# Performance work log

Measured on AMD Instinct MI355X. Metric: run time of the kernel, lower is better.

The kernel has to match this reference:

```python
import jax, jax.numpy as jnp
import numpy as np

GRID = 128  # grid_size from init_kwargs


def _splat(coords2, alpha, feats):
    """Alpha-weighted splat of per-point features onto a GRIDxGRID plane.
    coords2: [N,2] normalized coords in [-1,1]; alpha: [N]; feats: [N,C].
    Returns [C, GRID, GRID].
    """
    g = ((coords2 * 0.5 + 0.5) * (GRID - 1)).astype(jnp.int32)  # trunc like torch .long()
    g = jnp.clip(g, 0, GRID - 1)
    idx = g[:, 0] * GRID + g[:, 1]  # [N]
    num = jax.ops.segment_sum(feats * alpha[:, None], idx, num_segments=GRID * GRID)  # [G2,C]
    den = jnp.maximum(jax.ops.segment_sum(alpha, idx, num_segments=GRID * GRID), 1e-6)  # [G2]
    C = feats.shape[-1]
    return (num / den[:, None]).T.reshape(C, GRID, GRID)


def setup_inputs() -> dict:
    key = jax.random.key(0)
    k1, _ = jax.random.split(key)
    B, N, C = 4, 131072, 196
    GS_feats = jax.random.normal(k1, (B, N, C), dtype=jnp.float32)
    scene_bounds = jnp.arange(6, dtype=jnp.float32)  # (0,1,2,3,4,5) -> unit extents
    return {"GS_feats": GS_feats, "scene_bounds": scene_bounds}


def reference(GS_feats, scene_bounds):
    lo = scene_bounds[jnp.array([0, 2, 4])]  # [3]
    hi = scene_bounds[jnp.array([1, 3, 5])]  # [3]
    coords_n = 2.0 * (GS_feats[..., :3] - lo) / (hi - lo) - 1.0  # [B,N,3]
    feats = jnp.concatenate([coords_n, GS_feats[..., 3:]], axis=-1)  # [B,N,C]
    alpha = jax.nn.sigmoid(feats[..., 3])  # [B,N]
    # plane coord pairs: xy, xz, yz -> [B,3,N,2]
    plane_coords = jnp.stack(
        [coords_n[..., jnp.array([0, 1])],
         coords_n[..., jnp.array([0, 2])],
         coords_n[..., jnp.array([1, 2])]], axis=1)
    splat_planes = jax.vmap(_splat, in_axes=(0, None, None))  # over the 3 planes
    splat_batch = jax.vmap(splat_planes, in_axes=(0, 0, 0))   # over batch
    return splat_batch(plane_coords, alpha, feats)  # [B,3,C,GRID,GRID]
```

## Files before the change

kernel.cpp:

```cpp
#include <hip/hip_runtime.h>
#include <math.h>

#define GRID_SZ 128
#define NC 196
#define NC4 49
#define G2 (GRID_SZ*GRID_SZ)
#define BPB 64
#define SLOTS 128
#define SLOTF 200
#define AW 16


__device__ __forceinline__ void lds_flush(float* __restrict__ tbl, int tag,
                                          float v0, float v1, float v2, float v3,
                                          float d, int lane, bool l4) {
    float* slot = tbl + tag * SLOTF;
    atomicAdd(slot + lane, v0);
    atomicAdd(slot + 64 + lane, v1);
    atomicAdd(slot + 128 + lane, v2);
    if (l4) atomicAdd(slot + 192 + lane, v3);
    if (lane == 4) atomicAdd(slot + 196, d);
}

__global__ __launch_bounds__(1024, 1) void lds_accum_kernel(
    const float* __restrict__ gs, const float* __restrict__ sb,
    float* __restrict__ nw, float* __restrict__ dn,
    float* __restrict__ tblout, int N) {
    __shared__ float tbl[SLOTS * SLOTF];

    const int tid = threadIdx.x;
    const int lane = tid & 63;
    const int widx = tid >> 6;

    for (int i = tid; i < SLOTS * SLOTF; i += 1024) tbl[i] = 0.f;
    __syncthreads();

    const int b = blockIdx.x / BPB;
    const int blk = blockIdx.x % BPB;
    const int strip = N / BPB;
    const int cnt = strip / AW;
    const long long p0 = (long long)b * N + (long long)blk * strip
                       + (long long)widx * cnt;

    const float lo0 = sb[0], hi0 = sb[1];
    const float lo1 = sb[2], hi1 = sb[3];
    const float lo2 = sb[4], hi2 = sb[5];
    const float s0 = 2.0f / (hi0 - lo0);
    const float s1 = 2.0f / (hi1 - lo1);
    const float s2 = 2.0f / (hi2 - lo2);

    const float* rows = gs + (size_t)p0 * NC;
    const bool l4 = (lane < 4);

    #define LOADP(J, V0, V1, V2, V3)                                   \
        {                                                              \
            const float* r_ = rows + (size_t)(J) * NC;                 \
            V0 = r_[lane];                                             \
            V1 = r_[64 + lane];                                        \
            V2 = r_[128 + lane];                                       \
            V3 = l4 ? r_[192 + lane] : 0.f;                            \
        }

    float a0, a1, a2, a3, b0, b1, b2, b3;
    float c0_, c1_, c2_, c3_, d0, d1, d2, d3;
    {
        const int i1 = (cnt > 1) ? 1 : 0;
        const int i2 = (cnt > 2) ? 2 : 0;
        const int i3 = (cnt > 3) ? 3 : 0;
        LOADP(0, a0, a1, a2, a3);
        LOADP(i1, b0, b1, b2, b3);
        LOADP(i2, c0_, c1_, c2_, c3_);
        LOADP(i3, d0, d1, d2, d3);
    }

    float z0 = 0.f, z1 = 0.f, z2 = 0.f, z3 = 0.f, zd = 0.f;
    float y0 = 0.f, y1 = 0.f, y2 = 0.f, y3 = 0.f, yd = 0.f;
    int ctag = -1;
    float cc0 = 0.f, cc1 = 0.f, cc2 = 0.f, cc3 = 0.f, ccd = 0.f;

    #define CONSUME(V0, V1, V2, V3)                                          \
        {                                                                    \
            const float hx = __shfl(V0, 0);                                  \
            const float hy = __shfl(V0, 1);                                  \
            const float hz = __shfl(V0, 2);                                  \
            const float hw = __shfl(V0, 3);                                  \
            const float cnx = (hx - lo0) * s0 - 1.0f;                        \
            const float cny = (hy - lo1) * s1 - 1.0f;                        \
            const float cnz = (hz - lo2) * s2 - 1.0f;                        \
            int gx = (int)((cnx * 0.5f + 0.5f) * 127.0f);                    \
            int gy = (int)((cny * 0.5f + 0.5f) * 127.0f);                    \
            int gz = (int)((cnz * 0.5f + 0.5f) * 127.0f);                    \
            gx = min(127, max(0, gx));                                       \
            gy = min(127, max(0, gy));                                       \
            gz = min(127, max(0, gz));                                       \
            const float alpha = 1.0f / (1.0f + __expf(-hw));                 \
            float v0 = V0;                                                   \
            if (lane == 0) v0 = cnx;                                         \
            else if (lane == 1) v0 = cny;                                    \
            else if (lane == 2) v0 = cnz;                                    \
            const float av0 = v0 * alpha;                                    \
            const float av1 = (V1) * alpha;                                  \
            const float av2 = (V2) * alpha;                                  \
            const float av3 = (V3) * alpha;                                  \
            if ((gy | gz) == 0) {                                            \
                if (gx == 0) {                                               \
                    z0 += av0; z1 += av1; z2 += av2; z3 += av3; zd += alpha; \
                } else if (gx == 127) {                                      \
                    y0 += av0; y1 += av1; y2 += av2; y3 += av3; yd += alpha; \
                } else if (gx == ctag) {                                     \
                    cc0 += av0; cc1 += av1; cc2 += av2; cc3 += av3;          \
                    ccd += alpha;                                            \
                } else {                                                     \
                    if (ctag > 0)                                            \
                        lds_flush(tbl, ctag, cc0, cc1, cc2, cc3, ccd,        \
                                  lane, l4);                                 \
                    ctag = gx;                                               \
                    cc0 = av0; cc1 = av1; cc2 = av2; cc3 = av3;              \
                    ccd = alpha;                                             \
                }                                                            \
            } else {                                                         \
                const int cells[3] = { gx * GRID_SZ + gy, gx * GRID_SZ + gz, \
                                       gy * GRID_SZ + gz };                  \
                _Pragma("unroll")                                            \
                for (int p = 0; p < 3; ++p) {                                \
                    const int bin = (b * 3 + p) * G2 + cells[p];             \
                    float* dst = nw + (size_t)bin * NC;                      \
                    unsafeAtomicAdd(dst + lane, av0);                        \
                    unsafeAtomicAdd(dst + 64 + lane, av1);                   \
                    unsafeAtomicAdd(dst + 128 + lane, av2);                  \
                    if (l4) unsafeAtomicAdd(dst + 192 + lane, av3);          \
                    if (lane == 4) unsafeAtomicAdd(dn + bin, alpha);         \
                }                                                            \
            }                                                                \
        }

    for (int j = 0; j < cnt; j += 4) {
        float e0, e1, e2, e3, f0, f1, f2, f3;
        float g0, g1, g2, g3, h0, h1, h2, h3;
        const int j4 = (j + 4 < cnt) ? j + 4 : cnt - 1;
        const int j5 = (j + 5 < cnt) ? j + 5 : cnt - 1;
        const int j6 = (j + 6 < cnt) ? j + 6 : cnt - 1;
        const int j7 = (j + 7 < cnt) ? j + 7 : cnt - 1;
        LOADP(j4, e0, e1, e2, e3);
        LOADP(j5, f0, f1, f2, f3);
        LOADP(j6, g0, g1, g2, g3);
        LOADP(j7, h0, h1, h2, h3);

        CONSUME(a0, a1, a2, a3);
        CONSUME(b0, b1, b2, b3);
        CONSUME(c0_, c1_, c2_, c3_);
        CONSUME(d0, d1, d2, d3);

        a0 = e0; a1 = e1; a2 = e2; a3 = e3;
        b0 = f0; b1 = f1; b2 = f2; b3 = f3;
        c0_ = g0; c1_ = g1; c2_ = g2; c3_ = g3;
        d0 = h0; d1 = h1; d2 = h2; d3 = h3;
    }
    #undef CONSUME
    #undef LOADP

    if (ctag > 0) lds_flush(tbl, ctag, cc0, cc1, cc2, cc3, ccd, lane, l4);
    lds_flush(tbl, 127, y0, y1, y2, y3, yd, lane, l4);
    lds_flush(tbl, 0, z0, z1, z2, z3, zd, lane, l4);

    __syncthreads();
    for (int i = tid; i < SLOTS * SLOTF; i += 1024) {
        const int s = i / SLOTF;
        const int f = i - s * SLOTF;
        tblout[(((size_t)b * SLOTS + s) * BPB + blk) * SLOTF + f] = tbl[i];
    }
}


__global__ __launch_bounds__(256) void table_reduce_kernel(
    const float* __restrict__ tblout,
    float* __restrict__ nw, float* __restrict__ dn, int B) {
    const int lane = threadIdx.x & 63;
    const int w = blockIdx.x * 4 + (threadIdx.x >> 6);
    if (w >= B * SLOTS) return;
    const int b = w >> 7;
    const int gx = w & 127;
    const bool l4 = (lane < 4);

    const float* base = tblout + ((size_t)(b * SLOTS + gx) * BPB) * SLOTF;
    float a0 = 0.f, a1 = 0.f, a2 = 0.f, a3 = 0.f, den = 0.f;
    for (int r = 0; r < BPB; ++r) {
        const float* rec = base + (size_t)r * SLOTF;
        a0 += rec[lane];
        a1 += rec[64 + lane];
        a2 += rec[128 + lane];
        if (l4) a3 += rec[192 + lane];
        if (lane == 4) den += rec[196];
    }

    const int cells[3] = { gx * GRID_SZ, gx * GRID_SZ, 0 };
    #pragma unroll
    for (int p = 0; p < 3; ++p) {
        const int bin = (b * 3 + p) * G2 + cells[p];
        float* dst = nw + (size_t)bin * NC;
        unsafeAtomicAdd(dst + lane, a0);
        unsafeAtomicAdd(dst + 64 + lane, a1);
        unsafeAtomicAdd(dst + 128 + lane, a2);
        if (l4) unsafeAtomicAdd(dst + 192 + lane, a3);
        if (lane == 4) unsafeAtomicAdd(dn + bin, den);
    }
}


#define TCELLS 64
__global__ __launch_bounds__(256) void xpose_kernel(const float* __restrict__ nw,
                                                    const float* __restrict__ dn,
                                                    float* __restrict__ out) {
    __shared__ float tile[TCELLS][197];
    __shared__ float dinv[TCELLS];
    const int t = threadIdx.x;
    const int pg = blockIdx.x >> 8;
    const int c0 = (blockIdx.x & 255) * TCELLS;

    const float* src = nw + ((size_t)pg * G2 + c0) * NC;
    for (int i = t; i < TCELLS * NC4; i += 256) {
        const int cell = i / NC4;
        const int cp = i - cell * NC4;
        float4 v = ((const float4*)(src + (size_t)cell * NC))[cp];
        float* dst = &tile[cell][cp * 4];
        dst[0] = v.x; dst[1] = v.y; dst[2] = v.z; dst[3] = v.w;
    }
    if (t < TCELLS) dinv[t] = 1.0f / fmaxf(dn[pg * G2 + c0 + t], 1e-6f);
    __syncthreads();

    float* obase = out + (size_t)pg * NC * G2 + c0;
    for (int i = t; i < TCELLS * NC; i += 256) {
        const int c = i >> 6;
        const int cell = i & 63;
        obase[(size_t)c * G2 + cell] = tile[cell][c] * dinv[cell];
    }
}


__global__ void zero_kernel(float4* __restrict__ p, long long n4) {
    long long i = (long long)blockIdx.x * blockDim.x + threadIdx.x;
    long long stride = (long long)gridDim.x * blockDim.x;
    const float4 z = make_float4(0.f, 0.f, 0.f, 0.f);
    for (; i < n4; i += stride) p[i] = z;
}


struct Slot { int tag; float den; float4 acc; };

__device__ __forceinline__ void slot_flush(const Slot& s, float* __restrict__ out,
                                           float* __restrict__ den,
                                           size_t outPlaneBase, int denPlaneBase, int lane) {
    if (s.tag < 0) return;
    if (lane < NC4) {
        size_t base = outPlaneBase + (size_t)(4 * lane) * G2 + (size_t)s.tag;
        unsafeAtomicAdd(out + base,                s.acc.x);
        unsafeAtomicAdd(out + base + (size_t)G2,   s.acc.y);
        unsafeAtomicAdd(out + base + (size_t)2*G2, s.acc.z);
        unsafeAtomicAdd(out + base + (size_t)3*G2, s.acc.w);
    }
    if (lane == 0) unsafeAtomicAdd(den + denPlaneBase + s.tag, s.den);
}

__device__ __forceinline__ void plane_acc(Slot& a, Slot& b, int cell, float alpha,
                                          const float4& av,
                                          float* __restrict__ out, float* __restrict__ den,
                                          size_t outPlaneBase, int denPlaneBase, int lane) {
    if (cell == a.tag) {
        a.acc.x += av.x; a.acc.y += av.y; a.acc.z += av.z; a.acc.w += av.w; a.den += alpha;
    } else if (cell == b.tag) {
        b.acc.x += av.x; b.acc.y += av.y; b.acc.z += av.z; b.acc.w += av.w; b.den += alpha;
    } else {
        if (b.den > a.den) { Slot t = a; a = b; b = t; }
        slot_flush(b, out, den, outPlaneBase, denPlaneBase, lane);
        b.tag = cell; b.den = alpha; b.acc = av;
    }
}

__global__ __launch_bounds__(256) void splat_kernel(
    const float* __restrict__ gs, const float* __restrict__ sb,
    float* __restrict__ out, float* __restrict__ den, int B, int N, int ppw) {
    const int lane = threadIdx.x & 63;
    const long long wave = (long long)blockIdx.x * (blockDim.x >> 6) + (threadIdx.x >> 6);
    const long long totalPts = (long long)B * N;
    long long start = wave * ppw;
    if (start >= totalPts) return;
    long long end = start + ppw;
    if (end > totalPts) end = totalPts;
    const int bb = (int)(start / N);

    const float lo0 = sb[0], hi0 = sb[1];
    const float lo1 = sb[2], hi1 = sb[3];
    const float lo2 = sb[4], hi2 = sb[5];
    const float s0 = 2.0f / (hi0 - lo0);
    const float s1 = 2.0f / (hi1 - lo1);
    const float s2 = 2.0f / (hi2 - lo2);

    const size_t ob0 = ((size_t)(bb * 3 + 0) * NC) * G2;
    const size_t ob1 = ((size_t)(bb * 3 + 1) * NC) * G2;
    const size_t ob2 = ((size_t)(bb * 3 + 2) * NC) * G2;
    const int db0 = (bb * 3 + 0) * G2;
    const int db1 = (bb * 3 + 1) * G2;
    const int db2 = (bb * 3 + 2) * G2;

    const float4 f40 = make_float4(0.f, 0.f, 0.f, 0.f);
    Slot a0{-1,0.f,f40}, t0{-1,0.f,f40}, a1{-1,0.f,f40}, t1{-1,0.f,f40},
         a2{-1,0.f,f40}, t2{-1,0.f,f40};

    const float4* rows = (const float4*)gs;
    const float4* r0 = rows + (size_t)start * NC4;
    float4 v = (lane < NC4) ? r0[lane] : f40;
    float4 h = r0[0];

    for (long long i = start; i < end; ++i) {
        float4 vn = f40, hn = f40;
        if (i + 1 < end) {
            const float4* rn = rows + (size_t)(i + 1) * NC4;
            vn = (lane < NC4) ? rn[lane] : f40;
            hn = rn[0];
        }
        const float cnx = (h.x - lo0) * s0 - 1.0f;
        const float cny = (h.y - lo1) * s1 - 1.0f;
        const float cnz = (h.z - lo2) * s2 - 1.0f;
        int gx = (int)((cnx * 0.5f + 0.5f) * 127.0f);
        int gy = (int)((cny * 0.5f + 0.5f) * 127.0f);
        int gz = (int)((cnz * 0.5f + 0.5f) * 127.0f);
        gx = min(127, max(0, gx)); gy = min(127, max(0, gy)); gz = min(127, max(0, gz));
        const int cxy = __builtin_amdgcn_readfirstlane(gx * GRID_SZ + gy);
        const int cxz = __builtin_amdgcn_readfirstlane(gx * GRID_SZ + gz);
        const int cyz = __builtin_amdgcn_readfirstlane(gy * GRID_SZ + gz);
        const float alpha = 1.0f / (1.0f + __expf(-h.w));
        float4 vv = v;
        if (lane == 0) { vv.x = cnx; vv.y = cny; vv.z = cnz; }
        const float4 av = make_float4(vv.x*alpha, vv.y*alpha, vv.z*alpha, vv.w*alpha);
        plane_acc(a0, t0, cxy, alpha, av, out, den, ob0, db0, lane);
        plane_acc(a1, t1, cxz, alpha, av, out, den, ob1, db1, lane);
        plane_acc(a2, t2, cyz, alpha, av, out, den, ob2, db2, lane);
        v = vn; h = hn;
    }
    slot_flush(a0, out, den, ob0, db0, lane);
    slot_flush(t0, out, den, ob0, db0, lane);
    slot_flush(a1, out, den, ob1, db1, lane);
    slot_flush(t1, out, den, ob1, db1, lane);
    slot_flush(a2, out, den, ob2, db2, lane);
    slot_flush(t2, out, den, ob2, db2, lane);
}

__global__ void normalize_kernel(float* __restrict__ out, const float* __restrict__ den,
                                 int total4) {
    int idx = blockIdx.x * blockDim.x + threadIdx.x;
    const int stride = gridDim.x * blockDim.x;
    for (; idx < total4; idx += stride) {
        float4 v = ((float4*)out)[idx];
        const int e = idx * 4;
        const int cell = e & (G2 - 1);
        const int bp = e / (NC * G2);
        const float4 d = *(const float4*)(den + bp * G2 + cell);
        v.x /= fmaxf(d.x, 1e-6f);
        v.y /= fmaxf(d.y, 1e-6f);
        v.z /= fmaxf(d.z, 1e-6f);
        v.w /= fmaxf(d.w, 1e-6f);
        ((float4*)out)[idx] = v;
    }
}


extern "C" void kernel_launch(void* const* d_in, const int* in_sizes, int n_in,
                              void* d_out, int out_size, void* d_ws, size_t ws_size,
                              hipStream_t stream) {
    const float* gs = (const float*)d_in[0];
    const float* sb = (const float*)d_in[1];
    float* out = (float*)d_out;

    const int B = out_size / (3 * NC * G2);
    const int N = (int)((long long)in_sizes[0] / ((long long)B * NC));
    const int NB = B * 3 * G2;

    const size_t nwF = (size_t)NB * NC;
    const size_t dnF = (size_t)NB;
    const size_t tblF = (size_t)B * SLOTS * BPB * SLOTF;
    size_t off = 0;
    const size_t o_nw = off;    off += nwF * 4;
    const size_t o_dn = off;    off += dnF * 4;
    const size_t o_tbl = off;   off += tblF * 4;
    const size_t need = off;

    if (ws_size >= need && (N % (BPB * AW)) == 0 && B >= 1) {
        char* ws = (char*)d_ws;
        float* nw = (float*)(ws + o_nw);
        float* dn = (float*)(ws + o_dn);
        float* tblout = (float*)(ws + o_tbl);

        zero_kernel<<<4096, 256, 0, stream>>>((float4*)nw,
                                              (long long)(nwF + dnF) / 4);

        const int aBlocks = B * BPB;
        lds_accum_kernel<<<aBlocks, 1024, 0, stream>>>(gs, sb, nw, dn, tblout, N);

        const int rWaves = B * SLOTS;
        const int rBlocks = (rWaves + 3) / 4;
        table_reduce_kernel<<<rBlocks, 256, 0, stream>>>(tblout, nw, dn, B);

        const int xblocks = B * 3 * (G2 / TCELLS);
        xpose_kernel<<<xblocks, 256, 0, stream>>>(nw, dn, out);
    } else {
        float* den = (float*)d_ws;
        const long long out4 = (long long)out_size / 4;
        const long long den4 = (long long)dnF / 4;
        const int ppw = 64;
        const long long waves = ((long long)B * N) / ppw;
        const int blocks = (int)((waves + 3) / 4);
        zero_kernel<<<2048, 256, 0, stream>>>((float4*)out, out4);
        zero_kernel<<<256, 256, 0, stream>>>((float4*)den, den4);
        splat_kernel<<<blocks, 256, 0, stream>>>(gs, sb, out, den, B, N, ppw);
        normalize_kernel<<<4096, 256, 0, stream>>>(out, den, (int)out4);
    }
}
```

Before: 351.4 us.

## Defer rare global-atomic points to per-wave LDS list processed after streaming loop

The main streaming loop now keeps only the common path, where points land on the gy=gz=0 row and are accumulated in registers or LDS. Points needing global atomics are recorded as indices in a per-wave LDS list and replayed after the loop. Alpha and the weighted values are computed only on the common path, and prefetch pointer arithmetic is simplified, which keeps the hot loop lean. The list holds 128 entries per wave and has no overflow check, so correctness relies on few such points per wave. The initial loads also assume cnt is at least 4.

```diff
diff --git a/kernel.cpp b/kernel.cpp
--- a/kernel.cpp
+++ b/kernel.cpp
@@ -27,6 +27,7 @@
     float* __restrict__ nw, float* __restrict__ dn,
     float* __restrict__ tblout, int N) {
     __shared__ float tbl[SLOTS * SLOTF];
+    __shared__ unsigned short tlist[AW * 128];
 
     const int tid = threadIdx.x;
     const int lane = tid & 63;
@@ -52,33 +53,28 @@
     const float* rows = gs + (size_t)p0 * NC;
     const bool l4 = (lane < 4);
 
-    #define LOADP(J, V0, V1, V2, V3)                                   \
+    #define LOADG(P, K, V0, V1, V2, V3)                                \
         {                                                              \
-            const float* r_ = rows + (size_t)(J) * NC;                 \
-            V0 = r_[lane];                                             \
-            V1 = r_[64 + lane];                                        \
-            V2 = r_[128 + lane];                                       \
-            V3 = l4 ? r_[192 + lane] : 0.f;                            \
+            V0 = (P)[(K) * NC + lane];                                 \
+            V1 = (P)[(K) * NC + 64 + lane];                            \
+            V2 = (P)[(K) * NC + 128 + lane];                           \
+            V3 = l4 ? (P)[(K) * NC + 192 + lane] : 0.f;                \
         }
 
     float a0, a1, a2, a3, b0, b1, b2, b3;
     float c0_, c1_, c2_, c3_, d0, d1, d2, d3;
-    {
-        const int i1 = (cnt > 1) ? 1 : 0;
-        const int i2 = (cnt > 2) ? 2 : 0;
-        const int i3 = (cnt > 3) ? 3 : 0;
-        LOADP(0, a0, a1, a2, a3);
-        LOADP(i1, b0, b1, b2, b3);
-        LOADP(i2, c0_, c1_, c2_, c3_);
-        LOADP(i3, d0, d1, d2, d3);
-    }
+    LOADG(rows, 0, a0, a1, a2, a3);
+    LOADG(rows, 1, b0, b1, b2, b3);
+    LOADG(rows, 2, c0_, c1_, c2_, c3_);
+    LOADG(rows, 3, d0, d1, d2, d3);
 
     float z0 = 0.f, z1 = 0.f, z2 = 0.f, z3 = 0.f, zd = 0.f;
     float y0 = 0.f, y1 = 0.f, y2 = 0.f, y3 = 0.f, yd = 0.f;
     int ctag = -1;
     float cc0 = 0.f, cc1 = 0.f, cc2 = 0.f, cc3 = 0.f, ccd = 0.f;
-
-    #define CONSUME(V0, V1, V2, V3)                                          \
+    int tcnt = 0;
+
+    #define CONSUME(V0, V1, V2, V3, JIDX)                                    \
         {                                                                    \
             const float hx = __shfl(V0, 0);                                  \
             const float hy = __shfl(V0, 1);                                  \
@@ -93,16 +89,16 @@
             gx = min(127, max(0, gx));                                       \
             gy = min(127, max(0, gy));                                       \
             gz = min(127, max(0, gz));                                       \
-            const float alpha = 1.0f / (1.0f + __expf(-hw));                 \
-            float v0 = V0;                                                   \
-            if (lane == 0) v0 = cnx;                                         \
-            else if (lane == 1) v0 = cny;                                    \
-            else if (lane == 2) v0 = cnz;                                    \
-            const float av0 = v0 * alpha;                                    \
-            const float av1 = (V1) * alpha;                                  \
-            const float av2 = (V2) * alpha;                                  \
-            const float av3 = (V3) * alpha;                                  \
             if ((gy | gz) == 0) {                                            \
+                const float alpha = 1.0f / (1.0f + __expf(-hw));             \
+                float v0 = V0;                                               \
+                if (lane == 0) v0 = cnx;                                     \
+                else if (lane == 1) v0 = cny;                                \
+                else if (lane == 2) v0 = cnz;                                \
+                const float av0 = v0 * alpha;                                \
+                const float av1 = (V1) * alpha;                              \
+                const float av2 = (V2) * alpha;                              \
+                const float av3 = (V3) * alpha;                              \
                 if (gx == 0) {                                               \
                     z0 += av0; z1 += av1; z2 += av2; z3 += av3; zd += alpha; \
                 } else if (gx == 127) {                                      \
@@ -119,49 +115,80 @@
                     ccd = alpha;                                             \
                 }                                                            \
             } else {                                                         \
-                const int cells[3] = { gx * GRID_SZ + gy, gx * GRID_SZ + gz, \
-                                       gy * GRID_SZ + gz };                  \
-                _Pragma("unroll")                                            \
-                for (int p = 0; p < 3; ++p) {                                \
-                    const int bin = (b * 3 + p) * G2 + cells[p];             \
-                    float* dst = nw + (size_t)bin * NC;                      \
-                    unsafeAtomicAdd(dst + lane, av0);                        \
-                    unsafeAtomicAdd(dst + 64 + lane, av1);                   \
-                    unsafeAtomicAdd(dst + 128 + lane, av2);                  \
-                    if (l4) unsafeAtomicAdd(dst + 192 + lane, av3);          \
-                    if (lane == 4) unsafeAtomicAdd(dn + bin, alpha);         \
-                }                                                            \
+                if (lane == 0)                                               \
+                    tlist[widx * 128 + tcnt] = (unsigned short)(JIDX);       \
+                ++tcnt;                                                      \
             }                                                                \
         }
 
+    const float* pc = rows;
     for (int j = 0; j < cnt; j += 4) {
+        const float* pp = (j + 4 < cnt) ? pc + 4 * NC : pc;
         float e0, e1, e2, e3, f0, f1, f2, f3;
         float g0, g1, g2, g3, h0, h1, h2, h3;
-        const int j4 = (j + 4 < cnt) ? j + 4 : cnt - 1;
-        const int j5 = (j + 5 < cnt) ? j + 5 : cnt - 1;
-        const int j6 = (j + 6 < cnt) ? j + 6 : cnt - 1;
-        const int j7 = (j + 7 < cnt) ? j + 7 : cnt - 1;
-        LOADP(j4, e0, e1, e2, e3);
-        LOADP(j5, f0, f1, f2, f3);
-        LOADP(j6, g0, g1, g2, g3);
-        LOADP(j7, h0, h1, h2, h3);
-
-        CONSUME(a0, a1, a2, a3);
-        CONSUME(b0, b1, b2, b3);
-        CONSUME(c0_, c1_, c2_, c3_);
-        CONSUME(d0, d1, d2, d3);
+        LOADG(pp, 0, e0, e1, e2, e3);
+        LOADG(pp, 1, f0, f1, f2, f3);
+        LOADG(pp, 2, g0, g1, g2, g3);
+        LOADG(pp, 3, h0, h1, h2, h3);
+
+        CONSUME(a0, a1, a2, a3, j + 0);
+        CONSUME(b0, b1, b2, b3, j + 1);
+        CONSUME(c0_, c1_, c2_, c3_, j + 2);
+        CONSUME(d0, d1, d2, d3, j + 3);
 
         a0 = e0; a1 = e1; a2 = e2; a3 = e3;
         b0 = f0; b1 = f1; b2 = f2; b3 = f3;
         c0_ = g0; c1_ = g1; c2_ = g2; c3_ = g3;
         d0 = h0; d1 = h1; d2 = h2; d3 = h3;
+        pc = pp;
     }
     #undef CONSUME
-    #undef LOADP
 
     if (ctag > 0) lds_flush(tbl, ctag, cc0, cc1, cc2, cc3, ccd, lane, l4);
     lds_flush(tbl, 127, y0, y1, y2, y3, yd, lane, l4);
     lds_flush(tbl, 0, z0, z1, z2, z3, zd, lane, l4);
+
+    for (int t = 0; t < tcnt; ++t) {
+        const int j = (int)tlist[widx * 128 + t];
+        const float* r_ = rows + (size_t)j * NC;
+        float t0, t1, t2, t3;
+        LOADG(r_, 0, t0, t1, t2, t3);
+        const float hx = __shfl(t0, 0);
+        const float hy = __shfl(t0, 1);
+        const float hz = __shfl(t0, 2);
+        const float hw = __shfl(t0, 3);
+        const float cnx = (hx - lo0) * s0 - 1.0f;
+        const float cny = (hy - lo1) * s1 - 1.0f;
+        const float cnz = (hz - lo2) * s2 - 1.0f;
+        int gx = (int)((cnx * 0.5f + 0.5f) * 127.0f);
+        int gy = (int)((cny * 0.5f + 0.5f) * 127.0f);
+        int gz = (int)((cnz * 0.5f + 0.5f) * 127.0f);
+        gx = min(127, max(0, gx));
+        gy = min(127, max(0, gy));
+        gz = min(127, max(0, gz));
+        const float alpha = 1.0f / (1.0f + __expf(-hw));
+        float v0 = t0;
+        if (lane == 0) v0 = cnx;
+        else if (lane == 1) v0 = cny;
+        else if (lane == 2) v0 = cnz;
+        const float av0 = v0 * alpha;
+        const float av1 = t1 * alpha;
+        const float av2 = t2 * alpha;
+        const float av3 = t3 * alpha;
+        const int cells[3] = { gx * GRID_SZ + gy, gx * GRID_SZ + gz,
+                               gy * GRID_SZ + gz };
+        #pragma unroll
+        for (int p = 0; p < 3; ++p) {
+            const int bin = (b * 3 + p) * G2 + cells[p];
+            float* dst = nw + (size_t)bin * NC;
+            unsafeAtomicAdd(dst + lane, av0);
+            unsafeAtomicAdd(dst + 64 + lane, av1);
+            unsafeAtomicAdd(dst + 128 + lane, av2);
+            if (l4) unsafeAtomicAdd(dst + 192 + lane, av3);
+            if (lane == 4) unsafeAtomicAdd(dn + bin, alpha);
+        }
+    }
+    #undef LOADG
 
     __syncthreads();
     for (int i = tid; i < SLOTS * SLOTF; i += 1024) {
```

Result: no change. 358.3 us (+2.0%).
